# Optimization experiments

Measured on AMD Instinct MI355X. Metric: run time of the kernel, lower is better.

Reference implementation:

```python
import jax, jax.numpy as jnp
import numpy as np

B, C, H, W = 4, 256, 64, 64
CQ = C // 8


def setup_inputs() -> dict:
    key = jax.random.key(0)
    ks = jax.random.split(key, 8)
    s = 0.02
    return {
        "x": jax.random.normal(ks[0], (B, C, H, W), dtype=jnp.float32),
        "Wq": jax.random.normal(ks[1], (CQ, C), dtype=jnp.float32) * s,
        "bq": jax.random.normal(ks[2], (CQ,), dtype=jnp.float32) * s,
        "Wk": jax.random.normal(ks[3], (CQ, C), dtype=jnp.float32) * s,
        "bk": jax.random.normal(ks[4], (CQ,), dtype=jnp.float32) * s,
        "Wv": jax.random.normal(ks[5], (C, C), dtype=jnp.float32) * s,
        "bv": jax.random.normal(ks[6], (C,), dtype=jnp.float32) * s,
        "gamma": jax.random.normal(ks[7], (1,), dtype=jnp.float32) * s,
    }


def reference(x, Wq, bq, Wk, bk, Wv, bv, gamma):
    b, c, h, w = x.shape
    n = h * w
    xf = x.reshape(b, c, n)  # [B,C,N]; 1x1 conv == channel matmul
    q = jnp.einsum("oc,bcn->bno", Wq, xf) + bq  # [B,N,CQ]
    k = jnp.einsum("oc,bcn->bon", Wk, xf) + bk[:, None]  # [B,CQ,N]
    v = jnp.einsum("oc,bcn->bno", Wv, xf) + bv  # [B,N,C]
    attn = jnp.einsum("bnd,bdm->bnm", q, k)  # [B,N,N], unscaled
    attn = jax.nn.softmax(attn, axis=1)  # non-standard axis (over rows)
    out = jnp.einsum("bnm,bmc->bnc", attn, v)  # [B,N,C]
    out = out.transpose(0, 2, 1).reshape(b, c, h, w)
    return gamma * out + x
```

## Files before the change

### kernel.cpp

```cpp
#include <hip/hip_runtime.h>

#define B_ 4
#define C_ 256
#define N_ 4096
#define LOG2E 1.44269504088896340736f

typedef __attribute__((ext_vector_type(8))) short bf16x8;
typedef __attribute__((ext_vector_type(4))) float f32x4;

static __device__ __forceinline__ unsigned short f2bf(float f) {
    unsigned u = __builtin_bit_cast(unsigned, f);
    u += 0x7fffu + ((u >> 16) & 1u);
    return (unsigned short)(u >> 16);
}

static __device__ __forceinline__ float fexp2(float x) {
#if __has_builtin(__builtin_amdgcn_exp2f)
    return __builtin_amdgcn_exp2f(x);
#else
    return exp2f(x);
#endif
}

__global__ void k0_wprep(const float* __restrict__ Wq, const float* __restrict__ Wk,
                         const float* __restrict__ Wv, float* __restrict__ WqkT,
                         float* __restrict__ WvT) {
    int t = blockIdx.x * 256 + threadIdx.x;
    if (t < 256 * 64) {
        int c = t >> 6, o = t & 63;
        WqkT[t] = (o < 32) ? Wq[o * C_ + c] * LOG2E : Wk[(o - 32) * C_ + c];
    }
    int t2 = t - 256 * 64;
    if (t2 >= 0 && t2 < 256 * 256) {
        int cp = t2 >> 8, c = t2 & 255;
        WvT[t2] = Wv[c * C_ + cp];
    }
}

__global__ __launch_bounds__(256) void k1_qk(const float* __restrict__ x,
        const float* __restrict__ WqkT, const float* __restrict__ bq,
        const float* __restrict__ bk, unsigned short* __restrict__ qb,
        unsigned short* __restrict__ ktb) {
    __shared__ float red[4][64][33];
    int b = blockIdx.z, isk = blockIdx.y;
    int l = threadIdx.x & 63, v = threadIdx.x >> 6;
    int n = blockIdx.x * 64 + l;
    float acc[32];
#pragma unroll
    for (int o = 0; o < 32; ++o) acc[o] = 0.0f;
    const float* xp = x + (size_t)b * C_ * N_ + n;
    const float* wbase = WqkT + (isk ? 32 : 0);
#pragma unroll 4
    for (int c = 64 * v; c < 64 * v + 64; ++c) {
        float xv = xp[(size_t)c * N_];
        const float4* wr4 = (const float4*)(wbase + c * 64);
#pragma unroll
        for (int o4 = 0; o4 < 8; ++o4) {
            float4 wv = wr4[o4];
            acc[4 * o4 + 0] += wv.x * xv;
            acc[4 * o4 + 1] += wv.y * xv;
            acc[4 * o4 + 2] += wv.z * xv;
            acc[4 * o4 + 3] += wv.w * xv;
        }
    }
#pragma unroll
    for (int o = 0; o < 32; ++o) red[v][l][o] = acc[o];
    __syncthreads();
    int nl = threadIdx.x & 63, ob = (threadIdx.x >> 6) * 8;
    const float* bias = isk ? bk : bq;
    float bs = isk ? 1.0f : LOG2E;
    unsigned pk[4];
#pragma unroll
    for (int i = 0; i < 4; ++i) {
        int o0 = ob + 2 * i, o1 = ob + 2 * i + 1;
        float v0 = red[0][nl][o0] + red[1][nl][o0] + red[2][nl][o0] + red[3][nl][o0] + bias[o0] * bs;
        float v1 = red[0][nl][o1] + red[1][nl][o1] + red[2][nl][o1] + red[3][nl][o1] + bias[o1] * bs;
        pk[i] = (unsigned)f2bf(v0) | ((unsigned)f2bf(v1) << 16);
    }
    unsigned short* dst = (isk ? ktb : qb) + ((size_t)b * N_ + blockIdx.x * 64 + nl) * 32 + ob;
    *(uint4*)dst = make_uint4(pk[0], pk[1], pk[2], pk[3]);
}

__global__ __launch_bounds__(512) void k2_stats(const unsigned short* __restrict__ qb,
        const unsigned short* __restrict__ ktb, float* __restrict__ Wcol) {
    __shared__ float red[64][33];
    int b = blockIdx.y;
    int m0 = blockIdx.x * 64;
    int lane = threadIdx.x & 63, w = threadIdx.x >> 6;
    int r16 = lane & 15, g = lane >> 4;
    const unsigned short* kb = ktb + ((size_t)b * N_ + m0 + r16) * 32 + 8 * g;
    bf16x8 kf0 = *(const bf16x8*)(kb);
    bf16x8 kf1 = *(const bf16x8*)(kb + 16 * 32);
    bf16x8 kf2 = *(const bf16x8*)(kb + 32 * 32);
    bf16x8 kf3 = *(const bf16x8*)(kb + 48 * 32);
    float z0 = 0, z1 = 0, z2 = 0, z3 = 0;
    const unsigned short* qbase = qb + ((size_t)b * N_ + w * 512 + r16) * 32 + 8 * g;
#pragma unroll 2
    for (int n0 = 0; n0 < 512; n0 += 16) {
        bf16x8 qf = *(const bf16x8*)(qbase + (size_t)n0 * 32);
        f32x4 d0 = __builtin_amdgcn_mfma_f32_16x16x32_bf16(qf, kf0, (f32x4){0, 0, 0, 0}, 0, 0, 0);
        f32x4 d1 = __builtin_amdgcn_mfma_f32_16x16x32_bf16(qf, kf1, (f32x4){0, 0, 0, 0}, 0, 0, 0);
        f32x4 d2 = __builtin_amdgcn_mfma_f32_16x16x32_bf16(qf, kf2, (f32x4){0, 0, 0, 0}, 0, 0, 0);
        f32x4 d3 = __builtin_amdgcn_mfma_f32_16x16x32_bf16(qf, kf3, (f32x4){0, 0, 0, 0}, 0, 0, 0);
        z0 += fexp2(d0[0]) + fexp2(d0[1]) + fexp2(d0[2]) + fexp2(d0[3]);
        z1 += fexp2(d1[0]) + fexp2(d1[1]) + fexp2(d1[2]) + fexp2(d1[3]);
        z2 += fexp2(d2[0]) + fexp2(d2[1]) + fexp2(d2[2]) + fexp2(d2[3]);
        z3 += fexp2(d3[0]) + fexp2(d3[1]) + fexp2(d3[2]) + fexp2(d3[3]);
    }
    red[r16][4 * w + g] = z0;
    red[16 + r16][4 * w + g] = z1;
    red[32 + r16][4 * w + g] = z2;
    red[48 + r16][4 * w + g] = z3;
    __syncthreads();
    if (threadIdx.x < 64) {
        float s = 0;
#pragma unroll
        for (int i = 0; i < 32; ++i) s += red[threadIdx.x][i];
        Wcol[(size_t)b * N_ + m0 + threadIdx.x] = 1.0f / s;
    }
}

__global__ __launch_bounds__(256) void k3_v(const float* __restrict__ x,
        const float* __restrict__ WvT, const float* __restrict__ bv,
        const float* __restrict__ Wcol, unsigned short* __restrict__ vtb) {
    int b = blockIdx.z;
    int c0 = blockIdx.y * 32;
    int m = blockIdx.x * 256 + threadIdx.x;
    const float* xp = x + (size_t)b * C_ * N_ + m;
    float acc[32];
#pragma unroll
    for (int j = 0; j < 32; ++j) acc[j] = bv[c0 + j];
#pragma unroll 4
    for (int cp = 0; cp < C_; ++cp) {
        float xv = xp[(size_t)cp * N_];
        const float4* wr4 = (const float4*)(WvT + cp * C_ + c0);
#pragma unroll
        for (int j4 = 0; j4 < 8; ++j4) {
            float4 wv = wr4[j4];
            acc[4 * j4 + 0] += wv.x * xv;
            acc[4 * j4 + 1] += wv.y * xv;
            acc[4 * j4 + 2] += wv.z * xv;
            acc[4 * j4 + 3] += wv.w * xv;
        }
    }
    float wm = Wcol[(size_t)b * N_ + m];
#pragma unroll
    for (int j = 0; j < 32; ++j)
        vtb[((size_t)b * C_ + c0 + j) * N_ + m] = f2bf(acc[j] * wm);
}

__global__ __launch_bounds__(512) void k4_pv(const float* __restrict__ x,
        const unsigned short* __restrict__ qb, const unsigned short* __restrict__ ktb,
        const unsigned short* __restrict__ vtb,
        const float* __restrict__ gamma, float* __restrict__ out) {
    __shared__ unsigned short Pl[2][64 * 64];
    int b = blockIdx.y;
    int n0 = blockIdx.x * 64;
    int lane = threadIdx.x & 63, w = threadIdx.x >> 6;
    int ms = w >> 1, wn = w & 1;
    int r16 = lane & 15, g = lane >> 4;
    int swz = (r16 & 7) << 4;

    const unsigned short* qbp = qb + ((size_t)b * N_ + n0 + 32 * wn + r16) * 32 + 8 * g;
    bf16x8 qf0 = *(const bf16x8*)(qbp);
    bf16x8 qf1 = *(const bf16x8*)(qbp + 16 * 32);
    const unsigned short* kbp = ktb + ((size_t)b * N_ + 16 * ms + r16) * 32 + 8 * g;
    const unsigned short* vbp = vtb + ((size_t)b * C_ + 32 * w + r16) * N_ + 8 * g;

    char* pwbase = (char*)&Pl[0][0] + (32 * wn + r16) * 128 + ((32 * ms + 8 * g) ^ swz);

    f32x4 acc[4][2];
#pragma unroll
    for (int i = 0; i < 4; ++i)
#pragma unroll
        for (int j = 0; j < 2; ++j) acc[i][j] = (f32x4){0, 0, 0, 0};

    bf16x8 ka = *(const bf16x8*)(kbp);
    bf16x8 vb[2][2], vbn[2][2];
#pragma unroll
    for (int cs = 0; cs < 2; ++cs)
#pragma unroll
        for (int ks = 0; ks < 2; ++ks)
            vb[cs][ks] = *(const bf16x8*)(vbp + (size_t)cs * 16 * N_ + 32 * ks);
    {
        f32x4 s0 = __builtin_amdgcn_mfma_f32_16x16x32_bf16(ka, qf0, (f32x4){0, 0, 0, 0}, 0, 0, 0);
        f32x4 s1 = __builtin_amdgcn_mfma_f32_16x16x32_bf16(ka, qf1, (f32x4){0, 0, 0, 0}, 0, 0, 0);
        unsigned a0 = (unsigned)f2bf(fexp2(s0[0])) | ((unsigned)f2bf(fexp2(s0[1])) << 16);
        unsigned a1 = (unsigned)f2bf(fexp2(s0[2])) | ((unsigned)f2bf(fexp2(s0[3])) << 16);
        unsigned a2 = (unsigned)f2bf(fexp2(s1[0])) | ((unsigned)f2bf(fexp2(s1[1])) << 16);
        unsigned a3 = (unsigned)f2bf(fexp2(s1[2])) | ((unsigned)f2bf(fexp2(s1[3])) << 16);
        *(uint2*)(pwbase) = make_uint2(a0, a1);
        *(uint2*)(pwbase + 16 * 128) = make_uint2(a2, a3);
    }
    __syncthreads();

#pragma unroll 2
    for (int t = 0; t < 64; ++t) {
        int cbuf = t & 1;
        bf16x8 kan = ka;
        if (t < 63) {
            size_t m1 = (size_t)(t + 1) * 64;
            kan = *(const bf16x8*)(kbp + m1 * 32);
#pragma unroll
            for (int cs = 0; cs < 2; ++cs)
#pragma unroll
                for (int ks = 0; ks < 2; ++ks)
                    vbn[cs][ks] = *(const bf16x8*)(vbp + (size_t)cs * 16 * N_ + m1 + 32 * ks);
        }
        const char* prd = (const char*)&Pl[cbuf][0] + r16 * 128;
        bf16x8 pa[4][2];
#pragma unroll
        for (int ns = 0; ns < 4; ++ns)
#pragma unroll
            for (int ks = 0; ks < 2; ++ks)
                pa[ns][ks] = *(const bf16x8*)(prd + ns * 16 * 128 + ((64 * ks + 16 * g) ^ swz));
#pragma unroll
        for (int ns = 0; ns < 4; ++ns)
#pragma unroll
            for (int cs = 0; cs < 2; ++cs)
#pragma unroll
                for (int ks = 0; ks < 2; ++ks)
                    acc[ns][cs] = __builtin_amdgcn_mfma_f32_16x16x32_bf16(
                        pa[ns][ks], vb[cs][ks], acc[ns][cs], 0, 0, 0);
        if (t < 63) {
            f32x4 s0 = __builtin_amdgcn_mfma_f32_16x16x32_bf16(kan, qf0, (f32x4){0, 0, 0, 0}, 0, 0, 0);
            f32x4 s1 = __builtin_amdgcn_mfma_f32_16x16x32_bf16(kan, qf1, (f32x4){0, 0, 0, 0}, 0, 0, 0);
            unsigned a0 = (unsigned)f2bf(fexp2(s0[0])) | ((unsigned)f2bf(fexp2(s0[1])) << 16);
            unsigned a1 = (unsigned)f2bf(fexp2(s0[2])) | ((unsigned)f2bf(fexp2(s0[3])) << 16);
            unsigned a2 = (unsigned)f2bf(fexp2(s1[0])) | ((unsigned)f2bf(fexp2(s1[1])) << 16);
            unsigned a3 = (unsigned)f2bf(fexp2(s1[2])) | ((unsigned)f2bf(fexp2(s1[3])) << 16);
            char* pw = pwbase + (cbuf ^ 1) * 8192;
            *(uint2*)(pw) = make_uint2(a0, a1);
            *(uint2*)(pw + 16 * 128) = make_uint2(a2, a3);
        }
        __syncthreads();
        ka = kan;
#pragma unroll
        for (int cs = 0; cs < 2; ++cs)
#pragma unroll
            for (int ks = 0; ks < 2; ++ks) vb[cs][ks] = vbn[cs][ks];
    }

    float gm = gamma[0];
#pragma unroll
    for (int ns = 0; ns < 4; ++ns)
#pragma unroll
        for (int cs = 0; cs < 2; ++cs) {
            size_t c = 32 * w + 16 * cs + r16;
            size_t idx = ((size_t)b * C_ + c) * N_ + n0 + 16 * ns + 4 * g;
            float4 xv = *(const float4*)(x + idx);
            float4 o;
            o.x = gm * acc[ns][cs][0] + xv.x;
            o.y = gm * acc[ns][cs][1] + xv.y;
            o.z = gm * acc[ns][cs][2] + xv.z;
            o.w = gm * acc[ns][cs][3] + xv.w;
            *(float4*)(out + idx) = o;
        }
}

extern "C" void kernel_launch(void* const* d_in, const int* in_sizes, int n_in,
                              void* d_out, int out_size, void* d_ws, size_t ws_size,
                              hipStream_t stream) {
    const float* x = (const float*)d_in[0];
    const float* Wq = (const float*)d_in[1];
    const float* bq = (const float*)d_in[2];
    const float* Wk = (const float*)d_in[3];
    const float* bk = (const float*)d_in[4];
    const float* Wv = (const float*)d_in[5];
    const float* bv = (const float*)d_in[6];
    const float* gamma = (const float*)d_in[7];
    float* out = (float*)d_out;

    char* ws = (char*)d_ws;
    unsigned short* qb  = (unsigned short*)(ws);
    unsigned short* ktb = (unsigned short*)(ws + (1u << 20));
    unsigned short* vtb = (unsigned short*)(ws + (2u << 20));
    float* Wcol = (float*)(ws + (10u << 20));
    float* WqkT = (float*)(ws + (10u << 20) + (1u << 16));
    float* WvT  = (float*)(ws + (10u << 20) + (2u << 16));

    k0_wprep<<<320, 256, 0, stream>>>(Wq, Wk, Wv, WqkT, WvT);
    k1_qk<<<dim3(N_ / 64, 2, B_), 256, 0, stream>>>(x, WqkT, bq, bk, qb, ktb);
    k2_stats<<<dim3(N_ / 64, B_), 512, 0, stream>>>(qb, ktb, Wcol);
    k3_v<<<dim3(N_ / 256, C_ / 32, B_), 256, 0, stream>>>(x, WvT, bv, Wcol, vtb);
    k4_pv<<<dim3(N_ / 64, B_), 512, 0, stream>>>(x, qb, ktb, vtb, gamma, out);
}
```

Before: 252.5 us.

## Reassociate attention as (P·X)·Wv^T and project values afterwards with MFMA

```diff
diff --git a/kernel.cpp b/kernel.cpp
--- a/kernel.cpp
+++ b/kernel.cpp
@@ -22,40 +22,39 @@
 #endif
 }
 
+#define LDS_BARRIER() asm volatile("s_waitcnt lgkmcnt(0)\n\ts_barrier" ::: "memory")
+
 __global__ void k0_wprep(const float* __restrict__ Wq, const float* __restrict__ Wk,
                          const float* __restrict__ Wv, float* __restrict__ WqkT,
-                         float* __restrict__ WvT) {
+                         unsigned short* __restrict__ wvb) {
     int t = blockIdx.x * 256 + threadIdx.x;
     if (t < 256 * 64) {
         int c = t >> 6, o = t & 63;
         WqkT[t] = (o < 32) ? Wq[o * C_ + c] * LOG2E : Wk[(o - 32) * C_ + c];
     }
     int t2 = t - 256 * 64;
-    if (t2 >= 0 && t2 < 256 * 256) {
-        int cp = t2 >> 8, c = t2 & 255;
-        WvT[t2] = Wv[c * C_ + cp];
-    }
-}
-
-__global__ __launch_bounds__(256) void k1_qk(const float* __restrict__ x,
+    if (t2 >= 0 && t2 < 256 * 256) wvb[t2] = f2bf(Wv[t2]);
+}
+
+__global__ __launch_bounds__(256) void k1_qkx(const float* __restrict__ x,
         const float* __restrict__ WqkT, const float* __restrict__ bq,
         const float* __restrict__ bk, unsigned short* __restrict__ qb,
-        unsigned short* __restrict__ ktb) {
-    __shared__ float red[4][64][33];
-    int b = blockIdx.z, isk = blockIdx.y;
+        unsigned short* __restrict__ ktb, unsigned short* __restrict__ xb) {
+    __shared__ float red[4][64][64];
+    int b = blockIdx.y;
+    int n0 = blockIdx.x * 64;
     int l = threadIdx.x & 63, v = threadIdx.x >> 6;
-    int n = blockIdx.x * 64 + l;
-    float acc[32];
-#pragma unroll
-    for (int o = 0; o < 32; ++o) acc[o] = 0.0f;
-    const float* xp = x + (size_t)b * C_ * N_ + n;
-    const float* wbase = WqkT + (isk ? 32 : 0);
-#pragma unroll 4
+    const float* xp = x + (size_t)b * C_ * N_ + n0 + l;
+    unsigned short* xbp = xb + (size_t)b * C_ * N_ + n0 + l;
+    float acc[64];
+#pragma unroll
+    for (int o = 0; o < 64; ++o) acc[o] = 0.0f;
     for (int c = 64 * v; c < 64 * v + 64; ++c) {
         float xv = xp[(size_t)c * N_];
-        const float4* wr4 = (const float4*)(wbase + c * 64);
-#pragma unroll
-        for (int o4 = 0; o4 < 8; ++o4) {
+        xbp[(size_t)c * N_] = f2bf(xv);
+        const float4* wr4 = (const float4*)(WqkT + c * 64);
+#pragma unroll
+        for (int o4 = 0; o4 < 16; ++o4) {
             float4 wv = wr4[o4];
             acc[4 * o4 + 0] += wv.x * xv;
             acc[4 * o4 + 1] += wv.y * xv;
@@ -64,21 +63,25 @@
         }
     }
 #pragma unroll
-    for (int o = 0; o < 32; ++o) red[v][l][o] = acc[o];
+    for (int o = 0; o < 64; ++o) red[v][l][o] = acc[o];
     __syncthreads();
-    int nl = threadIdx.x & 63, ob = (threadIdx.x >> 6) * 8;
-    const float* bias = isk ? bk : bq;
-    float bs = isk ? 1.0f : LOG2E;
-    unsigned pk[4];
-#pragma unroll
-    for (int i = 0; i < 4; ++i) {
-        int o0 = ob + 2 * i, o1 = ob + 2 * i + 1;
-        float v0 = red[0][nl][o0] + red[1][nl][o0] + red[2][nl][o0] + red[3][nl][o0] + bias[o0] * bs;
-        float v1 = red[0][nl][o1] + red[1][nl][o1] + red[2][nl][o1] + red[3][nl][o1] + bias[o1] * bs;
-        pk[i] = (unsigned)f2bf(v0) | ((unsigned)f2bf(v1) << 16);
-    }
-    unsigned short* dst = (isk ? ktb : qb) + ((size_t)b * N_ + blockIdx.x * 64 + nl) * 32 + ob;
-    *(uint4*)dst = make_uint4(pk[0], pk[1], pk[2], pk[3]);
+    int n = threadIdx.x & 63, og = threadIdx.x >> 6;
+    int o0 = og * 16;
+    unsigned pk[8];
+#pragma unroll
+    for (int i = 0; i < 8; ++i) {
+        int oa = o0 + 2 * i, ob = oa + 1;
+        float va = red[0][n][oa] + red[1][n][oa] + red[2][n][oa] + red[3][n][oa];
+        float vb = red[0][n][ob] + red[1][n][ob] + red[2][n][ob] + red[3][n][ob];
+        if (og < 2) { va += bq[oa] * LOG2E; vb += bq[ob] * LOG2E; }
+        else        { va += bk[oa - 32];    vb += bk[ob - 32]; }
+        pk[i] = (unsigned)f2bf(va) | ((unsigned)f2bf(vb) << 16);
+    }
+    unsigned short* dst = (og < 2)
+        ? qb + ((size_t)b * N_ + n0 + n) * 32 + o0
+        : ktb + ((size_t)b * N_ + n0 + n) * 32 + (o0 - 32);
+    ((uint4*)dst)[0] = make_uint4(pk[0], pk[1], pk[2], pk[3]);
+    ((uint4*)dst)[1] = make_uint4(pk[4], pk[5], pk[6], pk[7]);
 }
 
 __global__ __launch_bounds__(512) void k2_stats(const unsigned short* __restrict__ qb,
@@ -120,40 +123,12 @@
     }
 }
 
-__global__ __launch_bounds__(256) void k3_v(const float* __restrict__ x,
-        const float* __restrict__ WvT, const float* __restrict__ bv,
-        const float* __restrict__ Wcol, unsigned short* __restrict__ vtb) {
-    int b = blockIdx.z;
-    int c0 = blockIdx.y * 32;
-    int m = blockIdx.x * 256 + threadIdx.x;
-    const float* xp = x + (size_t)b * C_ * N_ + m;
-    float acc[32];
-#pragma unroll
-    for (int j = 0; j < 32; ++j) acc[j] = bv[c0 + j];
-#pragma unroll 4
-    for (int cp = 0; cp < C_; ++cp) {
-        float xv = xp[(size_t)cp * N_];
-        const float4* wr4 = (const float4*)(WvT + cp * C_ + c0);
-#pragma unroll
-        for (int j4 = 0; j4 < 8; ++j4) {
-            float4 wv = wr4[j4];
-            acc[4 * j4 + 0] += wv.x * xv;
-            acc[4 * j4 + 1] += wv.y * xv;
-            acc[4 * j4 + 2] += wv.z * xv;
-            acc[4 * j4 + 3] += wv.w * xv;
-        }
-    }
-    float wm = Wcol[(size_t)b * N_ + m];
-#pragma unroll
-    for (int j = 0; j < 32; ++j)
-        vtb[((size_t)b * C_ + c0 + j) * N_ + m] = f2bf(acc[j] * wm);
-}
-
-__global__ __launch_bounds__(512) void k4_pv(const float* __restrict__ x,
-        const unsigned short* __restrict__ qb, const unsigned short* __restrict__ ktb,
-        const unsigned short* __restrict__ vtb,
-        const float* __restrict__ gamma, float* __restrict__ out) {
+__global__ __launch_bounds__(512) void k4_y(const unsigned short* __restrict__ qb,
+        const unsigned short* __restrict__ ktb, const unsigned short* __restrict__ xb,
+        const float* __restrict__ Wcol, unsigned short* __restrict__ Yt,
+        float* __restrict__ rowP) {
     __shared__ unsigned short Pl[2][64 * 64];
+    __shared__ float rpl[4][64];
     int b = blockIdx.y;
     int n0 = blockIdx.x * 64;
     int lane = threadIdx.x & 63, w = threadIdx.x >> 6;
@@ -165,7 +140,8 @@
     bf16x8 qf0 = *(const bf16x8*)(qbp);
     bf16x8 qf1 = *(const bf16x8*)(qbp + 16 * 32);
     const unsigned short* kbp = ktb + ((size_t)b * N_ + 16 * ms + r16) * 32 + 8 * g;
-    const unsigned short* vbp = vtb + ((size_t)b * C_ + 32 * w + r16) * N_ + 8 * g;
+    const unsigned short* xbp = xb + ((size_t)b * C_ + 32 * w + r16) * N_ + 8 * g;
+    const float* izp = Wcol + (size_t)b * N_ + 16 * ms + 4 * g;
 
     char* pwbase = (char*)&Pl[0][0] + (32 * wn + r16) * 128 + ((32 * ms + 8 * g) ^ swz);
 
@@ -174,38 +150,48 @@
     for (int i = 0; i < 4; ++i)
 #pragma unroll
         for (int j = 0; j < 2; ++j) acc[i][j] = (f32x4){0, 0, 0, 0};
+    float rp0 = 0.0f, rp1 = 0.0f;
 
     bf16x8 ka = *(const bf16x8*)(kbp);
-    bf16x8 vb[2][2], vbn[2][2];
+    bf16x8 xf[2][2], xfn[2][2];
 #pragma unroll
     for (int cs = 0; cs < 2; ++cs)
 #pragma unroll
         for (int ks = 0; ks < 2; ++ks)
-            vb[cs][ks] = *(const bf16x8*)(vbp + (size_t)cs * 16 * N_ + 32 * ks);
+            xf[cs][ks] = *(const bf16x8*)(xbp + (size_t)cs * 16 * N_ + 32 * ks);
+    float4 iz = *(const float4*)(izp);
     {
         f32x4 s0 = __builtin_amdgcn_mfma_f32_16x16x32_bf16(ka, qf0, (f32x4){0, 0, 0, 0}, 0, 0, 0);
         f32x4 s1 = __builtin_amdgcn_mfma_f32_16x16x32_bf16(ka, qf1, (f32x4){0, 0, 0, 0}, 0, 0, 0);
-        unsigned a0 = (unsigned)f2bf(fexp2(s0[0])) | ((unsigned)f2bf(fexp2(s0[1])) << 16);
-        unsigned a1 = (unsigned)f2bf(fexp2(s0[2])) | ((unsigned)f2bf(fexp2(s0[3])) << 16);
-        unsigned a2 = (unsigned)f2bf(fexp2(s1[0])) | ((unsigned)f2bf(fexp2(s1[1])) << 16);
-        unsigned a3 = (unsigned)f2bf(fexp2(s1[2])) | ((unsigned)f2bf(fexp2(s1[3])) << 16);
-        *(uint2*)(pwbase) = make_uint2(a0, a1);
-        *(uint2*)(pwbase + 16 * 128) = make_uint2(a2, a3);
-    }
-    __syncthreads();
+        float p00 = fexp2(s0[0]) * iz.x, p01 = fexp2(s0[1]) * iz.y;
+        float p02 = fexp2(s0[2]) * iz.z, p03 = fexp2(s0[3]) * iz.w;
+        float p10 = fexp2(s1[0]) * iz.x, p11 = fexp2(s1[1]) * iz.y;
+        float p12 = fexp2(s1[2]) * iz.z, p13 = fexp2(s1[3]) * iz.w;
+        rp0 += p00 + p01 + p02 + p03;
+        rp1 += p10 + p11 + p12 + p13;
+        *(uint2*)(pwbase) = make_uint2(
+            (unsigned)f2bf(p00) | ((unsigned)f2bf(p01) << 16),
+            (unsigned)f2bf(p02) | ((unsigned)f2bf(p03) << 16));
+        *(uint2*)(pwbase + 16 * 128) = make_uint2(
+            (unsigned)f2bf(p10) | ((unsigned)f2bf(p11) << 16),
+            (unsigned)f2bf(p12) | ((unsigned)f2bf(p13) << 16));
+    }
+    LDS_BARRIER();
 
 #pragma unroll 2
     for (int t = 0; t < 64; ++t) {
         int cbuf = t & 1;
         bf16x8 kan = ka;
+        float4 izn = iz;
         if (t < 63) {
             size_t m1 = (size_t)(t + 1) * 64;
             kan = *(const bf16x8*)(kbp + m1 * 32);
+            izn = *(const float4*)(izp + m1);
 #pragma unroll
             for (int cs = 0; cs < 2; ++cs)
 #pragma unroll
                 for (int ks = 0; ks < 2; ++ks)
-                    vbn[cs][ks] = *(const bf16x8*)(vbp + (size_t)cs * 16 * N_ + m1 + 32 * ks);
+                    xfn[cs][ks] = *(const bf16x8*)(xbp + (size_t)cs * 16 * N_ + m1 + 32 * ks);
         }
         const char* prd = (const char*)&Pl[cbuf][0] + r16 * 128;
         bf16x8 pa[4][2];
@@ -221,41 +207,108 @@
 #pragma unroll
                 for (int ks = 0; ks < 2; ++ks)
                     acc[ns][cs] = __builtin_amdgcn_mfma_f32_16x16x32_bf16(
-                        pa[ns][ks], vb[cs][ks], acc[ns][cs], 0, 0, 0);
+                        pa[ns][ks], xf[cs][ks], acc[ns][cs], 0, 0, 0);
         if (t < 63) {
             f32x4 s0 = __builtin_amdgcn_mfma_f32_16x16x32_bf16(kan, qf0, (f32x4){0, 0, 0, 0}, 0, 0, 0);
             f32x4 s1 = __builtin_amdgcn_mfma_f32_16x16x32_bf16(kan, qf1, (f32x4){0, 0, 0, 0}, 0, 0, 0);
-            unsigned a0 = (unsigned)f2bf(fexp2(s0[0])) | ((unsigned)f2bf(fexp2(s0[1])) << 16);
-            unsigned a1 = (unsigned)f2bf(fexp2(s0[2])) | ((unsigned)f2bf(fexp2(s0[3])) << 16);
-            unsigned a2 = (unsigned)f2bf(fexp2(s1[0])) | ((unsigned)f2bf(fexp2(s1[1])) << 16);
-            unsigned a3 = (unsigned)f2bf(fexp2(s1[2])) | ((unsigned)f2bf(fexp2(s1[3])) << 16);
+            float p00 = fexp2(s0[0]) * izn.x, p01 = fexp2(s0[1]) * izn.y;
+            float p02 = fexp2(s0[2]) * izn.z, p03 = fexp2(s0[3]) * izn.w;
+            float p10 = fexp2(s1[0]) * izn.x, p11 = fexp2(s1[1]) * izn.y;
+            float p12 = fexp2(s1[2]) * izn.z, p13 = fexp2(s1[3]) * izn.w;
+            rp0 += p00 + p01 + p02 + p03;
+            rp1 += p10 + p11 + p12 + p13;
             char* pw = pwbase + (cbuf ^ 1) * 8192;
-            *(uint2*)(pw) = make_uint2(a0, a1);
-            *(uint2*)(pw + 16 * 128) = make_uint2(a2, a3);
-        }
-        __syncthreads();
+            *(uint2*)(pw) = make_uint2(
+                (unsigned)f2bf(p00) | ((unsigned)f2bf(p01) << 16),
+                (unsigned)f2bf(p02) | ((unsigned)f2bf(p03) << 16));
+            *(uint2*)(pw + 16 * 128) = make_uint2(
+                (unsigned)f2bf(p10) | ((unsigned)f2bf(p11) << 16),
+                (unsigned)f2bf(p12) | ((unsigned)f2bf(p13) << 16));
+        }
+        LDS_BARRIER();
         ka = kan;
+        iz = izn;
 #pragma unroll
         for (int cs = 0; cs < 2; ++cs)
 #pragma unroll
-            for (int ks = 0; ks < 2; ++ks) vb[cs][ks] = vbn[cs][ks];
-    }
-
+            for (int ks = 0; ks < 2; ++ks) xf[cs][ks] = xfn[cs][ks];
+    }
+
+    rp0 += __shfl_xor(rp0, 16); rp0 += __shfl_xor(rp0, 32);
+    rp1 += __shfl_xor(rp1, 16); rp1 += __shfl_xor(rp1, 32);
+    if (g == 0) {
+        rpl[ms][32 * wn + r16] = rp0;
+        rpl[ms][32 * wn + 16 + r16] = rp1;
+    }
+    __syncthreads();
+    if (threadIdx.x < 64)
+        rowP[(size_t)b * N_ + n0 + threadIdx.x] =
+            rpl[0][threadIdx.x] + rpl[1][threadIdx.x] + rpl[2][threadIdx.x] + rpl[3][threadIdx.x];
+
+#pragma unroll
+    for (int ns = 0; ns < 4; ++ns)
+#pragma unroll
+        for (int cs = 0; cs < 2; ++cs) {
+            int cp = 32 * w + 16 * cs + r16;
+            f32x4 a = acc[ns][cs];
+#pragma unroll
+            for (int r = 0; r < 4; ++r) {
+                int n = n0 + 16 * ns + 4 * g + r;
+                Yt[((size_t)b * N_ + n) * C_ + cp] = f2bf(a[r]);
+            }
+        }
+}
+
+__global__ __launch_bounds__(256) void k5_out(const float* __restrict__ x,
+        const unsigned short* __restrict__ wvb, const unsigned short* __restrict__ Yt,
+        const float* __restrict__ rowP, const float* __restrict__ bv,
+        const float* __restrict__ gamma, float* __restrict__ out) {
+    int b = blockIdx.y;
+    int n0 = blockIdx.x * 32;
+    int lane = threadIdx.x & 63, w = threadIdx.x >> 6;
+    int r16 = lane & 15, g = lane >> 4;
+    const unsigned short* wvp = wvb + (64 * w + r16) * C_ + 8 * g;
+    const unsigned short* ytp = Yt + ((size_t)b * N_ + n0 + r16) * C_ + 8 * g;
+
+    f32x4 acc[4][2];
+#pragma unroll
+    for (int i = 0; i < 4; ++i)
+#pragma unroll
+        for (int j = 0; j < 2; ++j) acc[i][j] = (f32x4){0, 0, 0, 0};
+
+#pragma unroll
+    for (int kc = 0; kc < 8; ++kc) {
+        bf16x8 yf[2];
+#pragma unroll
+        for (int ns = 0; ns < 2; ++ns)
+            yf[ns] = *(const bf16x8*)(ytp + ns * 16 * C_ + kc * 32);
+#pragma unroll
+        for (int cs = 0; cs < 4; ++cs) {
+            bf16x8 wf = *(const bf16x8*)(wvp + cs * 16 * C_ + kc * 32);
+#pragma unroll
+            for (int ns = 0; ns < 2; ++ns)
+                acc[cs][ns] = __builtin_amdgcn_mfma_f32_16x16x32_bf16(
+                    wf, yf[ns], acc[cs][ns], 0, 0, 0);
+        }
+    }
     float gm = gamma[0];
-#pragma unroll
-    for (int ns = 0; ns < 4; ++ns)
-#pragma unroll
-        for (int cs = 0; cs < 2; ++cs) {
-            size_t c = 32 * w + 16 * cs + r16;
-            size_t idx = ((size_t)b * C_ + c) * N_ + n0 + 16 * ns + 4 * g;
-            float4 xv = *(const float4*)(x + idx);
-            float4 o;
-            o.x = gm * acc[ns][cs][0] + xv.x;
-            o.y = gm * acc[ns][cs][1] + xv.y;
-            o.z = gm * acc[ns][cs][2] + xv.z;
-            o.w = gm * acc[ns][cs][3] + xv.w;
-            *(float4*)(out + idx) = o;
-        }
+    float rpv[2];
+#pragma unroll
+    for (int ns = 0; ns < 2; ++ns) rpv[ns] = rowP[(size_t)b * N_ + n0 + 16 * ns + r16];
+#pragma unroll
+    for (int cs = 0; cs < 4; ++cs) {
+        float4 bvv = *(const float4*)(bv + 64 * w + 16 * cs + 4 * g);
+        float bva[4] = {bvv.x, bvv.y, bvv.z, bvv.w};
+#pragma unroll
+        for (int ns = 0; ns < 2; ++ns)
+#pragma unroll
+            for (int r = 0; r < 4; ++r) {
+                int c = 64 * w + 16 * cs + 4 * g + r;
+                int n = n0 + 16 * ns + r16;
+                size_t idx = ((size_t)b * C_ + c) * N_ + n;
+                out[idx] = gm * (acc[cs][ns][r] + rpv[ns] * bva[r]) + x[idx];
+            }
+    }
 }
 
 extern "C" void kernel_launch(void* const* d_in, const int* in_sizes, int n_in,
@@ -274,14 +327,16 @@
     char* ws = (char*)d_ws;
     unsigned short* qb  = (unsigned short*)(ws);
     unsigned short* ktb = (unsigned short*)(ws + (1u << 20));
-    unsigned short* vtb = (unsigned short*)(ws + (2u << 20));
-    float* Wcol = (float*)(ws + (10u << 20));
-    float* WqkT = (float*)(ws + (10u << 20) + (1u << 16));
-    float* WvT  = (float*)(ws + (10u << 20) + (2u << 16));
-
-    k0_wprep<<<320, 256, 0, stream>>>(Wq, Wk, Wv, WqkT, WvT);
-    k1_qk<<<dim3(N_ / 64, 2, B_), 256, 0, stream>>>(x, WqkT, bq, bk, qb, ktb);
+    unsigned short* xb  = (unsigned short*)(ws + (2u << 20));
+    unsigned short* Yt  = (unsigned short*)(ws + (10u << 20));
+    float* Wcol = (float*)(ws + (18u << 20));
+    float* WqkT = (float*)(ws + (18u << 20) + (1u << 16));
+    unsigned short* wvb = (unsigned short*)(ws + (18u << 20) + (2u << 16));
+    float* rowP = (float*)(ws + (18u << 20) + (4u << 16));
+
+    k0_wprep<<<320, 256, 0, stream>>>(Wq, Wk, Wv, WqkT, wvb);
+    k1_qkx<<<dim3(N_ / 64, B_), 256, 0, stream>>>(x, WqkT, bq, bk, qb, ktb, xb);
     k2_stats<<<dim3(N_ / 64, B_), 512, 0, stream>>>(qb, ktb, Wcol);
-    k3_v<<<dim3(N_ / 256, C_ / 32, B_), 256, 0, stream>>>(x, WvT, bv, Wcol, vtb);
-    k4_pv<<<dim3(N_ / 64, B_), 512, 0, stream>>>(x, qb, ktb, vtb, gamma, out);
-}
+    k4_y<<<dim3(N_ / 64, B_), 512, 0, stream>>>(qb, ktb, xb, Wcol, Yt, rowP);
+    k5_out<<<dim3(N_ / 32, B_), 256, 0, stream>>>(x, wvb, Yt, rowP, bv, gamma, out);
+}
```

After: 238.5 us. 5.5% less time.
